# Kernel tuning notes

Measured on AMD Instinct MI355X. Metric: run time of the kernel, lower is better.

The kernel has to match this reference:

```python
import jax, jax.numpy as jnp
import numpy as np


@jax.custom_vjp
def binarize(w):
    # Deterministic binarization: sign with ties (w==0) mapped to +1,
    # matching tf.where(w >= 0, 1.0, -1.0).
    return jnp.where(w >= 0, 1.0, -1.0).astype(w.dtype)


def _binarize_fwd(w):
    return binarize(w), w


def _binarize_bwd(w, g):
    # Straight-through estimator: pass grad where |w| < 1, else 0.
    return (jnp.where(jnp.abs(w) < 1.0, g, jnp.zeros_like(g)),)


binarize.defvjp(_binarize_fwd, _binarize_bwd)


def setup_inputs() -> dict:
    key = jax.random.key(0)
    kx, kw = jax.random.split(key)
    # NHWC activations
    x = jax.random.normal(kx, (32, 112, 112, 128), dtype=jnp.float32)
    # HWIO kernel (glorot-scale init so values straddle the +/- decision boundary)
    kernel = jax.random.normal(kw, (3, 3, 128, 256), dtype=jnp.float32) * 0.05
    return {"x": x, "kernel": kernel}


def reference(x, kernel):
    wb = binarize(kernel)  # [3,3,Cin,Cout] in {-1,+1}
    return jax.lax.conv_general_dilated(
        x, wb,
        window_strides=(1, 1),
        padding="SAME",
        dimension_numbers=("NHWC", "HWIO", "NHWC"),
    )
```

## Files before the change

### kernel.cpp

```cpp
#include <hip/hip_runtime.h>

typedef __attribute__((ext_vector_type(8))) short short8;
typedef __attribute__((ext_vector_type(4))) float f32x4;
typedef __attribute__((ext_vector_type(4))) unsigned short u16x4;
typedef __attribute__((ext_vector_type(8))) unsigned short u16x8;

#define H 112
#define W 112
#define HP 114
#define WP 114
#define CIN 128
#define COUT 256
#define NPIX (H * W)
#define NIMG 32
#define MTOT (NIMG * NPIX)
#define PADELEMS ((long)NIMG * HP * WP * CIN)
#define NSTEP 36

__device__ __forceinline__ unsigned short f2bf(float f) {
    unsigned int u = __builtin_bit_cast(unsigned int, f);
    u += 0x7FFFu + ((u >> 16) & 1u);
    return (unsigned short)(u >> 16);
}

__device__ __forceinline__ void gl2lds16(const void* g, void* l) {
    __builtin_amdgcn_global_load_lds(
        (const __attribute__((address_space(1))) unsigned int*)g,
        (__attribute__((address_space(3))) unsigned int*)l,
        16, 0, 0);
}

__global__ void binw3_kernel(const float* __restrict__ kw, unsigned short* __restrict__ bw) {
    int tid = blockIdx.x * 256 + threadIdx.x;
    int e    = tid & 7;
    int cout = (tid >> 3) & 255;
    int q    = (tid >> 11) & 3;
    int kc   = (tid >> 13) & 3;
    int tap  = tid >> 15;
    int cin  = kc * 32 + q * 8 + e;
    float w = kw[(tap * 128 + cin) * 256 + cout];
    bw[tid] = (w >= 0.0f) ? (unsigned short)0x3F80u : (unsigned short)0xBF80u;
}

__global__ void pad_kernel(const float* __restrict__ x, unsigned short* __restrict__ xp) {
    long tid = (long)blockIdx.x * 256 + threadIdx.x;
    if (tid >= PADELEMS / 8) return;
    int c8 = (int)(tid & 15);
    long rem = tid >> 4;
    int wp = (int)(rem % WP); rem /= WP;
    int hp = (int)(rem % HP);
    int n  = (int)(rem / HP);
    u16x8 v = {0, 0, 0, 0, 0, 0, 0, 0};
    if (hp >= 1 && hp <= H && wp >= 1 && wp <= W) {
        const float* s = x + (((long)(n * H + hp - 1) * W + (wp - 1)) * CIN + c8 * 8);
        f32x4 a = *(const f32x4*)s;
        f32x4 b = *(const f32x4*)(s + 4);
        v = (u16x8){ f2bf(a.x), f2bf(a.y), f2bf(a.z), f2bf(a.w),
                     f2bf(b.x), f2bf(b.y), f2bf(b.z), f2bf(b.w) };
    }
    *(u16x8*)(xp + tid * 8) = v;
}

__global__ __launch_bounds__(256, 4)
void conv8_kernel(const unsigned short* __restrict__ xp, const unsigned short* __restrict__ bw,
                  float* __restrict__ out) {
    __shared__ unsigned short As[2][4096];
    __shared__ unsigned short Bs[2][4096];

    const int tid = threadIdx.x;
    const int swz = (blockIdx.x & 7) * 784 + (blockIdx.x >> 3);
    const int bm = swz >> 1;
    const int bn = swz & 1;
    const int lane = tid & 63;
    const int wv = tid >> 6;
    const int wr = wv >> 1, wc = wv & 1;
    const int l15 = lane & 15;

    const int srow = tid & 127;
    const int sq = tid >> 7;
    {
        int p = bm * 128 + srow;
        int n0 = p / NPIX;
        int rem0 = p - n0 * NPIX;
        int oh0 = rem0 / W, ow0 = rem0 - oh0 * W;
        (void)oh0; (void)ow0;
    }
    int p0 = bm * 128 + srow;
    int n0 = p0 / NPIX;
    int rem0 = p0 - n0 * NPIX;
    int oh0 = rem0 / W, ow0 = rem0 - oh0 * W;
    const unsigned short* aptr = xp + (long)((n0 * HP + oh0 + 1) * WP + ow0 + 1) * CIN + sq * 8;
    const unsigned short* bptr = bw + (bn * 128 + srow) * 8 + sq * 2048;

#define STAGE(T, BUF) do {                                                      \
        const int _tap = (T) >> 2, _kc = (T) & 3;                               \
        const long _sh = (long)((_tap / 3 - 1) * WP + (_tap % 3 - 1)) * CIN     \
                         + _kc * 32;                                            \
        gl2lds16(aptr + _sh,      &As[BUF][tid * 8]);                           \
        gl2lds16(aptr + _sh + 16, &As[BUF][tid * 8 + 2048]);                    \
        gl2lds16(bptr + (T) * 8192,        &Bs[BUF][tid * 8]);                  \
        gl2lds16(bptr + (T) * 8192 + 4096, &Bs[BUF][tid * 8 + 2048]);           \
    } while (0)

    const int aoff = (lane >> 4) * 1024 + (wr * 64 + l15) * 8;
    const int boff = (lane >> 4) * 1024 + (wc * 64 + l15) * 8;

    f32x4 acc[4][4];
#pragma unroll
    for (int m = 0; m < 4; ++m)
#pragma unroll
        for (int n = 0; n < 4; ++n)
            acc[m][n] = (f32x4){0.f, 0.f, 0.f, 0.f};

    STAGE(0, 0);

#pragma unroll
    for (int t = 0; t < NSTEP; ++t) {
        const int buf = t & 1;
        if (t < NSTEP - 1) {
            STAGE(t + 1, buf ^ 1);
            asm volatile("s_waitcnt vmcnt(4)" ::: "memory");
        } else {
            asm volatile("s_waitcnt vmcnt(0)" ::: "memory");
        }
        __builtin_amdgcn_s_barrier();

        short8 afr[4], bfr[4];
#pragma unroll
        for (int n = 0; n < 4; ++n)
            bfr[n] = *(const short8*)&Bs[buf][boff + n * 128];
#pragma unroll
        for (int m = 0; m < 4; ++m)
            afr[m] = *(const short8*)&As[buf][aoff + m * 128];
        asm volatile("s_waitcnt lgkmcnt(0)" ::: "memory");
        __builtin_amdgcn_sched_barrier(0);
        __builtin_amdgcn_s_setprio(1);
#pragma unroll
        for (int m = 0; m < 4; ++m)
#pragma unroll
            for (int n = 0; n < 4; ++n)
                acc[m][n] = __builtin_amdgcn_mfma_f32_16x16x32_bf16(
                    afr[m], bfr[n], acc[m][n], 0, 0, 0);
        __builtin_amdgcn_s_setprio(0);
        __builtin_amdgcn_s_barrier();
    }
#undef STAGE

    const long row0 = (long)bm * 128 + wr * 64 + (lane >> 4) * 4;
    const int col = bn * 128 + wc * 64 + l15;
#pragma unroll
    for (int m = 0; m < 4; ++m)
#pragma unroll
        for (int n = 0; n < 4; ++n)
#pragma unroll
            for (int j = 0; j < 4; ++j)
                out[(row0 + m * 16 + j) * COUT + col + n * 16] = acc[m][n][j];
}

__global__ void binw_kernel(const float* __restrict__ kw, unsigned short* __restrict__ bw) {
    int tid = blockIdx.x * 256 + threadIdx.x;
    int cin5 = tid & 31;
    int cout = (tid >> 5) & 255;
    int kc4  = (tid >> 13) & 3;
    int tap  = tid >> 15;
    int cin  = kc4 * 32 + cin5;
    float w = kw[(tap * 128 + cin) * 256 + cout];
    bw[tid] = (w >= 0.0f) ? (unsigned short)0x3F80u : (unsigned short)0xBF80u;
}

__global__ __launch_bounds__(256, 2)
void conv_fallback_kernel(const float* __restrict__ x, const unsigned short* __restrict__ bw,
                          float* __restrict__ out) {
    __shared__ unsigned short As[128][40];
    __shared__ unsigned short Bs[128][40];
    const int tid = threadIdx.x;
    const int bm = blockIdx.x, bn = blockIdx.y;
    const int lane = tid & 63;
    const int wv = tid >> 6;
    const int wr = wv >> 1, wc = wv & 1;
    const int c4 = (tid & 7) * 4;
    const int rseg = tid >> 3;
    int ohs[4], ows[4], bases[4];
#pragma unroll
    for (int i = 0; i < 4; ++i) {
        int p = bm * 128 + rseg + i * 32;
        int n = p / NPIX;
        int rem = p - n * NPIX;
        int oh = rem / W, ow = rem - oh * W;
        ohs[i] = oh; ows[i] = ow;
        bases[i] = ((n * H + oh) * W + ow) * CIN;
    }
    f32x4 acc[4][4];
#pragma unroll
    for (int m = 0; m < 4; ++m)
#pragma unroll
        for (int n = 0; n < 4; ++n)
            acc[m][n] = (f32x4){0.f, 0.f, 0.f, 0.f};
    const int arow = wr * 64 + (lane & 15);
    const int brow = wc * 64 + (lane & 15);
    const int koff = (lane >> 4) * 8;
    for (int tap = 0; tap < 9; ++tap) {
        const int dh = tap / 3 - 1, dw = tap % 3 - 1;
        const int shift = (dh * W + dw) * CIN;
#pragma unroll
        for (int kc = 0; kc < 4; ++kc) {
            __syncthreads();
#pragma unroll
            for (int i = 0; i < 4; ++i) {
                int ih = ohs[i] + dh, iw = ows[i] + dw;
                bool valid = ((unsigned)ih < (unsigned)H) & ((unsigned)iw < (unsigned)W);
                f32x4 v = {0.f, 0.f, 0.f, 0.f};
                if (valid) v = *(const f32x4*)(x + bases[i] + shift + kc * 32 + c4);
                u16x4 s = { f2bf(v.x), f2bf(v.y), f2bf(v.z), f2bf(v.w) };
                *(u16x4*)&As[rseg + i * 32][c4] = s;
            }
            const unsigned short* bp = bw + tap * 32768 + kc * 8192 + bn * 4096;
#pragma unroll
            for (int j = 0; j < 2; ++j) {
                int idx = tid + j * 256;
                *(u16x8*)&Bs[idx >> 2][(idx & 3) * 8] = *(const u16x8*)(bp + (idx >> 2) * 32 + (idx & 3) * 8);
            }
            __syncthreads();
            short8 af[4], bfr[4];
#pragma unroll
            for (int m = 0; m < 4; ++m)
                af[m] = *(const short8*)&As[arow + m * 16][koff];
#pragma unroll
            for (int n = 0; n < 4; ++n)
                bfr[n] = *(const short8*)&Bs[brow + n * 16][koff];
#pragma unroll
            for (int m = 0; m < 4; ++m)
#pragma unroll
                for (int n = 0; n < 4; ++n)
                    acc[m][n] = __builtin_amdgcn_mfma_f32_16x16x32_bf16(af[m], bfr[n], acc[m][n], 0, 0, 0);
        }
    }
    const long row0 = (long)bm * 128 + wr * 64 + ((lane >> 4) * 4);
    const int col = bn * 128 + wc * 64 + (lane & 15);
#pragma unroll
    for (int m = 0; m < 4; ++m)
#pragma unroll
        for (int n = 0; n < 4; ++n)
#pragma unroll
            for (int j = 0; j < 4; ++j)
                out[(row0 + m * 16 + j) * COUT + col + n * 16] = acc[m][n][j];
}

extern "C" void kernel_launch(void* const* d_in, const int* in_sizes, int n_in,
                              void* d_out, int out_size, void* d_ws, size_t ws_size,
                              hipStream_t stream) {
    const float* x  = (const float*)d_in[0];
    const float* kw = (const float*)d_in[1];
    float* out = (float*)d_out;
    unsigned short* bw = (unsigned short*)d_ws;
    const size_t BW_BYTES = 9 * 4 * 4 * 256 * 8 * 2;
    const size_t PAD_BYTES = (size_t)PADELEMS * 2;

    if (ws_size >= BW_BYTES + PAD_BYTES) {
        binw3_kernel<<<(9 * 4 * 4 * 256 * 8) / 256, 256, 0, stream>>>(kw, bw);
        unsigned short* xp = (unsigned short*)((char*)d_ws + BW_BYTES);
        pad_kernel<<<(int)((PADELEMS / 8 + 255) / 256), 256, 0, stream>>>(x, xp);
        conv8_kernel<<<(MTOT / 128) * 2, 256, 0, stream>>>(xp, bw, out);
    } else {
        binw_kernel<<<(9 * 256 * 128) / 256, 256, 0, stream>>>(kw, bw);
        dim3 grid(MTOT / 128, COUT / 128);
        conv_fallback_kernel<<<grid, 256, 0, stream>>>(x, bw, out);
    }
}
```

Before: 396.1 us.

## Enlarge conv tile to 256x256 with 4-stage pipeline and channel-planar padded input

```diff
diff --git a/kernel.cpp b/kernel.cpp
--- a/kernel.cpp
+++ b/kernel.cpp
@@ -14,7 +14,8 @@
 #define NPIX (H * W)
 #define NIMG 32
 #define MTOT (NIMG * NPIX)
-#define PADELEMS ((long)NIMG * HP * WP * CIN)
+#define NPADPIX (NIMG * HP * WP)
+#define PADELEMS ((long)NPADPIX * CIN)
 #define NSTEP 36
 
 __device__ __forceinline__ unsigned short f2bf(float f) {
@@ -28,6 +29,13 @@
         (const __attribute__((address_space(1))) unsigned int*)g,
         (__attribute__((address_space(3))) unsigned int*)l,
         16, 0, 0);
+}
+
+__device__ __forceinline__ int pidx(int p) {
+    int n = p / NPIX;
+    int r = p - n * NPIX;
+    int oh = r / W, ow = r - oh * W;
+    return n * (HP * WP) + (oh + 1) * WP + ow + 1;
 }
 
 __global__ void binw3_kernel(const float* __restrict__ kw, unsigned short* __restrict__ bw) {
@@ -42,114 +50,106 @@
     bw[tid] = (w >= 0.0f) ? (unsigned short)0x3F80u : (unsigned short)0xBF80u;
 }
 
-__global__ void pad_kernel(const float* __restrict__ x, unsigned short* __restrict__ xp) {
-    long tid = (long)blockIdx.x * 256 + threadIdx.x;
-    if (tid >= PADELEMS / 8) return;
-    int c8 = (int)(tid & 15);
-    long rem = tid >> 4;
-    int wp = (int)(rem % WP); rem /= WP;
-    int hp = (int)(rem % HP);
-    int n  = (int)(rem / HP);
+__global__ void pad2_kernel(const float* __restrict__ x, unsigned short* __restrict__ xp) {
+    long s = (long)blockIdx.x * 256 + threadIdx.x;
+    if (s >= (long)16 * NPADPIX) return;
+    int c   = (int)(s / NPADPIX);
+    int pix = (int)(s - (long)c * NPADPIX);
+    int n  = pix / (HP * WP);
+    int r  = pix - n * (HP * WP);
+    int hp = r / WP, wp = r - hp * WP;
     u16x8 v = {0, 0, 0, 0, 0, 0, 0, 0};
     if (hp >= 1 && hp <= H && wp >= 1 && wp <= W) {
-        const float* s = x + (((long)(n * H + hp - 1) * W + (wp - 1)) * CIN + c8 * 8);
-        f32x4 a = *(const f32x4*)s;
-        f32x4 b = *(const f32x4*)(s + 4);
+        const float* src = x + (((long)(n * H + hp - 1) * W + (wp - 1)) * CIN + c * 8);
+        f32x4 a = *(const f32x4*)src;
+        f32x4 b = *(const f32x4*)(src + 4);
         v = (u16x8){ f2bf(a.x), f2bf(a.y), f2bf(a.z), f2bf(a.w),
                      f2bf(b.x), f2bf(b.y), f2bf(b.z), f2bf(b.w) };
     }
-    *(u16x8*)(xp + tid * 8) = v;
-}
-
-__global__ __launch_bounds__(256, 4)
-void conv8_kernel(const unsigned short* __restrict__ xp, const unsigned short* __restrict__ bw,
-                  float* __restrict__ out) {
-    __shared__ unsigned short As[2][4096];
-    __shared__ unsigned short Bs[2][4096];
+    *(u16x8*)(xp + s * 8) = v;
+}
+
+__global__ __launch_bounds__(512, 2)
+void conv12_kernel(const unsigned short* __restrict__ xp, const unsigned short* __restrict__ bw,
+                   float* __restrict__ out) {
+    __shared__ unsigned short As[4][4 * 256 * 8];
+    __shared__ unsigned short Bs[4][4 * 256 * 8];
 
     const int tid = threadIdx.x;
-    const int swz = (blockIdx.x & 7) * 784 + (blockIdx.x >> 3);
-    const int bm = swz >> 1;
-    const int bn = swz & 1;
+    const int bm = (blockIdx.x & 7) * 196 + (blockIdx.x >> 3);
     const int lane = tid & 63;
     const int wv = tid >> 6;
-    const int wr = wv >> 1, wc = wv & 1;
+    const int wr = wv >> 2;
+    const int wc = wv & 3;
     const int l15 = lane & 15;
 
-    const int srow = tid & 127;
-    const int sq = tid >> 7;
-    {
-        int p = bm * 128 + srow;
-        int n0 = p / NPIX;
-        int rem0 = p - n0 * NPIX;
-        int oh0 = rem0 / W, ow0 = rem0 - oh0 * W;
-        (void)oh0; (void)ow0;
-    }
-    int p0 = bm * 128 + srow;
-    int n0 = p0 / NPIX;
-    int rem0 = p0 - n0 * NPIX;
-    int oh0 = rem0 / W, ow0 = rem0 - oh0 * W;
-    const unsigned short* aptr = xp + (long)((n0 * HP + oh0 + 1) * WP + ow0 + 1) * CIN + sq * 8;
-    const unsigned short* bptr = bw + (bn * 128 + srow) * 8 + sq * 2048;
+    const int srow = tid & 255;
+    const int sp = tid >> 8;
+    const int apx = pidx(bm * 256 + srow);
+    const unsigned short* bwp = bw + srow * 8;
 
 #define STAGE(T, BUF) do {                                                      \
         const int _tap = (T) >> 2, _kc = (T) & 3;                               \
-        const long _sh = (long)((_tap / 3 - 1) * WP + (_tap % 3 - 1)) * CIN     \
-                         + _kc * 32;                                            \
-        gl2lds16(aptr + _sh,      &As[BUF][tid * 8]);                           \
-        gl2lds16(aptr + _sh + 16, &As[BUF][tid * 8 + 2048]);                    \
-        gl2lds16(bptr + (T) * 8192,        &Bs[BUF][tid * 8]);                  \
-        gl2lds16(bptr + (T) * 8192 + 4096, &Bs[BUF][tid * 8 + 2048]);           \
+        const int _tsh = (_tap / 3 - 1) * WP + (_tap % 3 - 1);                  \
+        gl2lds16(xp + ((long)(_kc * 4 + sp) * NPADPIX + apx + _tsh) * 8,        \
+                 &As[BUF][(sp * 256 + srow) * 8]);                              \
+        gl2lds16(xp + ((long)(_kc * 4 + sp + 2) * NPADPIX + apx + _tsh) * 8,    \
+                 &As[BUF][((sp + 2) * 256 + srow) * 8]);                        \
+        gl2lds16(bwp + (((_tap * 4 + _kc) * 4 + sp) * 256) * 8,                 \
+                 &Bs[BUF][(sp * 256 + srow) * 8]);                              \
+        gl2lds16(bwp + (((_tap * 4 + _kc) * 4 + sp + 2) * 256) * 8,             \
+                 &Bs[BUF][((sp + 2) * 256 + srow) * 8]);                        \
     } while (0)
 
-    const int aoff = (lane >> 4) * 1024 + (wr * 64 + l15) * 8;
-    const int boff = (lane >> 4) * 1024 + (wc * 64 + l15) * 8;
-
-    f32x4 acc[4][4];
-#pragma unroll
-    for (int m = 0; m < 4; ++m)
+    const int aoff = (lane >> 4) * 2048 + (wr * 128 + l15) * 8;
+    const int boff = (lane >> 4) * 2048 + (wc * 64 + l15) * 8;
+
+    f32x4 acc[8][4];
+#pragma unroll
+    for (int m = 0; m < 8; ++m)
 #pragma unroll
         for (int n = 0; n < 4; ++n)
             acc[m][n] = (f32x4){0.f, 0.f, 0.f, 0.f};
 
     STAGE(0, 0);
+    STAGE(1, 1);
+    STAGE(2, 2);
 
 #pragma unroll
     for (int t = 0; t < NSTEP; ++t) {
-        const int buf = t & 1;
-        if (t < NSTEP - 1) {
-            STAGE(t + 1, buf ^ 1);
+        const int buf = t & 3;
+        if (t < NSTEP - 2)
+            asm volatile("s_waitcnt vmcnt(8)" ::: "memory");
+        else if (t == NSTEP - 2)
             asm volatile("s_waitcnt vmcnt(4)" ::: "memory");
-        } else {
+        else
             asm volatile("s_waitcnt vmcnt(0)" ::: "memory");
-        }
         __builtin_amdgcn_s_barrier();
-
-        short8 afr[4], bfr[4];
+        if (t < NSTEP - 3) STAGE(t + 3, (t + 3) & 3);
+
+        short8 bfr[4], afr[8];
 #pragma unroll
         for (int n = 0; n < 4; ++n)
             bfr[n] = *(const short8*)&Bs[buf][boff + n * 128];
 #pragma unroll
-        for (int m = 0; m < 4; ++m)
+        for (int m = 0; m < 8; ++m)
             afr[m] = *(const short8*)&As[buf][aoff + m * 128];
-        asm volatile("s_waitcnt lgkmcnt(0)" ::: "memory");
-        __builtin_amdgcn_sched_barrier(0);
+
         __builtin_amdgcn_s_setprio(1);
 #pragma unroll
-        for (int m = 0; m < 4; ++m)
+        for (int m = 0; m < 8; ++m)
 #pragma unroll
             for (int n = 0; n < 4; ++n)
                 acc[m][n] = __builtin_amdgcn_mfma_f32_16x16x32_bf16(
                     afr[m], bfr[n], acc[m][n], 0, 0, 0);
         __builtin_amdgcn_s_setprio(0);
-        __builtin_amdgcn_s_barrier();
     }
 #undef STAGE
 
-    const long row0 = (long)bm * 128 + wr * 64 + (lane >> 4) * 4;
-    const int col = bn * 128 + wc * 64 + l15;
-#pragma unroll
-    for (int m = 0; m < 4; ++m)
+    const long row0 = (long)bm * 256 + wr * 128 + (lane >> 4) * 4;
+    const int col = wc * 64 + l15;
+#pragma unroll
+    for (int m = 0; m < 8; ++m)
 #pragma unroll
         for (int n = 0; n < 4; ++n)
 #pragma unroll
@@ -259,8 +259,9 @@
     if (ws_size >= BW_BYTES + PAD_BYTES) {
         binw3_kernel<<<(9 * 4 * 4 * 256 * 8) / 256, 256, 0, stream>>>(kw, bw);
         unsigned short* xp = (unsigned short*)((char*)d_ws + BW_BYTES);
-        pad_kernel<<<(int)((PADELEMS / 8 + 255) / 256), 256, 0, stream>>>(x, xp);
-        conv8_kernel<<<(MTOT / 128) * 2, 256, 0, stream>>>(xp, bw, out);
+        long slots = (long)16 * NPADPIX;
+        pad2_kernel<<<(int)((slots + 255) / 256), 256, 0, stream>>>(x, xp);
+        conv12_kernel<<<MTOT / 256, 512, 0, stream>>>(xp, bw, out);
     } else {
         binw_kernel<<<(9 * 256 * 128) / 256, 256, 0, stream>>>(kw, bw);
         dim3 grid(MTOT / 128, COUT / 128);
```

New measurement: 405.6 us. 2.4% more time.
